# Kernel tuning notes

Measured on AMD Instinct MI355X. Metric: run time of the kernel, lower is better.

The kernel has to match this reference:

```python
import jax, jax.numpy as jnp
import numpy as np

N_TABLES = 26
ROWS = 100001   # n + 1 per EmbeddingBag
D = 64          # m_spa
B = 8192
L = 4           # fixed pooling factor per bag


def setup_inputs() -> dict:
    key = jax.random.key(0)
    ks = jax.random.split(key, 16)
    inp = {}
    inp["dense_x"] = jax.random.normal(ks[0], (B, 13), dtype=jnp.float32)
    # offsets: bag k starts at k*L (fixed pooling factor), same for every table
    inp["lS_o"] = jnp.tile(jnp.arange(B, dtype=jnp.int64) * L, (N_TABLES, 1))
    inp["lS_i"] = jax.random.randint(ks[1], (N_TABLES, B * L), 0, 100000).astype(jnp.int64)
    # embedding tables, uniform(-r, r) with r = sqrt(2/(n+m))
    r = (2.0 / (100000 + D)) ** 0.5
    inp["emb_tables"] = jax.random.uniform(ks[2], (N_TABLES, ROWS, D), dtype=jnp.float32, minval=-r, maxval=r)
    def lin(k, n_in, n_out):
        k1, k2 = jax.random.split(k)
        w = jax.random.normal(k1, (n_out, n_in), dtype=jnp.float32) * (2.0 / n_in) ** 0.5
        b = jax.random.uniform(k2, (n_out,), dtype=jnp.float32, minval=-n_in**-0.5, maxval=n_in**-0.5)
        return w, b
    inp["bot_w0"], inp["bot_b0"] = lin(ks[3], 13, 512)
    inp["bot_w1"], inp["bot_b1"] = lin(ks[4], 512, 256)
    inp["bot_w2"], inp["bot_b2"] = lin(ks[5], 256, 64)
    inp["top_w0"], inp["top_b0"] = lin(ks[6], 415, 512)
    inp["top_w1"], inp["top_b1"] = lin(ks[7], 512, 256)
    inp["top_w2"], inp["top_b2"] = lin(ks[8], 256, 1)
    return inp


def _dlrm(dense_x, lS_o, lS_i, emb_tables,
          bot_w0, bot_b0, bot_w1, bot_b1, bot_w2, bot_b2,
          top_w0, top_b0, top_w1, top_b1, top_w2, top_b2):
    # bottom MLP: Linear+ReLU for every layer (sigmoid_bot=-1)
    x = jax.nn.relu(dense_x @ bot_w0.T + bot_b0)
    x = jax.nn.relu(x @ bot_w1.T + bot_b1)
    x = jax.nn.relu(x @ bot_w2.T + bot_b2)          # [B, D]
    # EmbeddingBag mean pooling per table (fixed bag length L encoded by lS_o)
    idx = lS_i.reshape(N_TABLES, B, L)
    gathered = jax.vmap(lambda tab, ix: tab[ix])(emb_tables, idx)  # [T, B, L, D]
    ly = gathered.mean(axis=2)                       # [T, B, D]
    # dot interaction: T_feat = cat([x]+ly) -> [B, 27, D]
    T_feat = jnp.concatenate([x[None], ly], axis=0).transpose(1, 0, 2)
    Z = jnp.einsum('bnd,bmd->bnm', T_feat, T_feat)   # [B, 27, 27]
    li, lj = np.tril_indices(N_TABLES + 1, -1)       # strict lower triangle (offset=0)
    Zflat = Z[:, li, lj]                             # [B, 351]
    R = jnp.concatenate([x, Zflat], axis=1)          # [B, 415]
    # top MLP: sigmoid_top=2 -> loop breaks before appending Sigmoid -> last layer linear
    z = jax.nn.relu(R @ top_w0.T + top_b0)
    z = jax.nn.relu(z @ top_w1.T + top_b1)
    z = z @ top_w2.T + top_b2                        # [B, 1]
    return z.reshape(-1)


def reference(dense_x, lS_o, lS_i, emb_tables,
              bot_w0, bot_b0, bot_w1, bot_b1, bot_w2, bot_b2,
              top_w0, top_b0, top_w1, top_b1, top_w2, top_b2):
    return _dlrm(dense_x, lS_o, lS_i, emb_tables,
                 bot_w0, bot_b0, bot_w1, bot_b1, bot_w2, bot_b2,
                 top_w0, top_b0, top_w1, top_b1, top_w2, top_b2)
```

## Files before the change

### kernel.cpp

```cpp
#include <hip/hip_runtime.h>
#include <hip/hip_bf16.h>

typedef short bf16x8 __attribute__((ext_vector_type(8)));
typedef float f32x4 __attribute__((ext_vector_type(4)));

__device__ __forceinline__ float relu_f(float v){ return v > 0.f ? v : 0.f; }

__device__ __forceinline__ f32x4 mfma16(bf16x8 a, bf16x8 b, f32x4 c){
  return __builtin_amdgcn_mfma_f32_16x16x32_bf16(a, b, c, 0, 0, 0);
}

__device__ __forceinline__ short bfbits(float v){
  __hip_bfloat16 h = __float2bfloat16(v);
  return *reinterpret_cast<short*>(&h);
}

__global__ __launch_bounds__(256) void prep(
    const float* __restrict__ X,  const float* __restrict__ bw0,
    const float* __restrict__ bb0, __hip_bfloat16* __restrict__ H,
    const float* __restrict__ bw1, __hip_bfloat16* __restrict__ w1b,
    const float* __restrict__ bw2, __hip_bfloat16* __restrict__ w2b,
    const float* __restrict__ tw0, __hip_bfloat16* __restrict__ tw0b,
    const float* __restrict__ tw1, __hip_bfloat16* __restrict__ tw1b){
  int blk = blockIdx.x;
  if (blk < 512){
    int n = threadIdx.x;
    int m0 = blk * 16;
    float w0[13], w1[13];
#pragma unroll
    for (int k = 0; k < 13; k++){ w0[k] = bw0[n*13 + k]; w1[k] = bw0[(n+256)*13 + k]; }
    float b0 = bb0[n], b1 = bb0[n + 256];
    for (int mi = 0; mi < 16; mi++){
      int m = m0 + mi;
      float a0 = b0, a1 = b1;
#pragma unroll
      for (int k = 0; k < 13; k++){
        float xv = X[m*13 + k];
        a0 += xv * w0[k]; a1 += xv * w1[k];
      }
      H[(size_t)m*512 + n]       = __float2bfloat16(relu_f(a0));
      H[(size_t)m*512 + n + 256] = __float2bfloat16(relu_f(a1));
    }
  } else if (blk < 1024){
    int i = (blk - 512)*256 + threadIdx.x;
    w1b[i] = __float2bfloat16(bw1[i]);
  } else if (blk < 1088){
    int i = (blk - 1024)*256 + threadIdx.x;
    w2b[i] = __float2bfloat16(bw2[i]);
  } else if (blk < 1920){
    int i = (blk - 1088)*256 + threadIdx.x;
    int r = i / 416, k = i - r*416;
    float v = (k < 415) ? tw0[r*415 + k] : 0.f;
    tw0b[i] = __float2bfloat16(v);
  } else {
    int i = (blk - 1920)*256 + threadIdx.x;
    tw1b[i] = __float2bfloat16(tw1[i]);
  }
}

template<int NT, int K>
__global__ __launch_bounds__(256) void gemm_br(const __hip_bfloat16* __restrict__ A,
    const __hip_bfloat16* __restrict__ W, const float* __restrict__ Bv,
    __hip_bfloat16* __restrict__ C, int N, int ldc){
  int lane = threadIdx.x & 63;
  int wave = blockIdx.x * 4 + (threadIdx.x >> 6);
  int ntiles = N / (16 * NT);
  int mi = wave / ntiles, ni = wave % ntiles;
  int row = lane & 15, quad = lane >> 4;
  const __hip_bfloat16* Ap = A + (size_t)(mi*16 + row) * K + quad*8;
  const __hip_bfloat16* Wp = W + (size_t)(ni*16*NT + row) * K + quad*8;
  f32x4 acc[NT];
#pragma unroll
  for (int t = 0; t < NT; t++) acc[t] = (f32x4){0.f, 0.f, 0.f, 0.f};
#pragma unroll
  for (int k = 0; k < K; k += 32){
    bf16x8 a = *(const bf16x8*)(Ap + k);
#pragma unroll
    for (int t = 0; t < NT; t++){
      bf16x8 b = *(const bf16x8*)(Wp + (size_t)t*16*K + k);
      acc[t] = mfma16(a, b, acc[t]);
    }
  }
#pragma unroll
  for (int t = 0; t < NT; t++){
    int n = ni*16*NT + t*16 + row;
    float bn = Bv[n];
#pragma unroll
    for (int r = 0; r < 4; r++){
      int m = mi*16 + quad*4 + r;
      C[(size_t)m*ldc + n] = __float2bfloat16(relu_f(acc[t][r] + bn));
    }
  }
}

__global__ __launch_bounds__(256) void embint(const int* __restrict__ I,
    const float* __restrict__ T, __hip_bfloat16* __restrict__ R){
  int b    = blockIdx.x * 4 + (threadIdx.x >> 6);
  int lane = threadIdx.x & 63;
  int row = lane & 15, quad = lane >> 4;
  __hip_bfloat16* Rb = R + (size_t)b * 416;

  int4 ix0 = {0,0,0,0}, ix1 = {0,0,0,0};
  if (row >= 1) ix0 = *(const int4*)(I + ((size_t)(row - 1) << 15) + (b << 2));
  if (row < 11) ix1 = *(const int4*)(I + ((size_t)(row + 15) << 15) + (b << 2));

  f32x4 a00 = {0,0,0,0}, a10 = {0,0,0,0}, a11 = {0,0,0,0};
#pragma unroll
  for (int k = 0; k < 64; k += 32){
    int ko = k + quad*8;
    bf16x8 f0, f1 = {0,0,0,0,0,0,0,0};
    if (row == 0){
      f0 = *(const bf16x8*)(Rb + ko);
    } else {
      const float* tb = T + (size_t)(row - 1) * 6400064ull + ko;
      float s[8] = {0,0,0,0,0,0,0,0};
      int idx[4] = {ix0.x, ix0.y, ix0.z, ix0.w};
#pragma unroll
      for (int l = 0; l < 4; l++){
        const float* p = tb + (size_t)idx[l]*64;
        float4 u = *(const float4*)p;
        float4 v = *(const float4*)(p + 4);
        s[0]+=u.x; s[1]+=u.y; s[2]+=u.z; s[3]+=u.w;
        s[4]+=v.x; s[5]+=v.y; s[6]+=v.z; s[7]+=v.w;
      }
#pragma unroll
      for (int j = 0; j < 8; j++) f0[j] = bfbits(s[j]*0.25f);
    }
    if (row < 11){
      const float* tb = T + (size_t)(row + 15) * 6400064ull + ko;
      float s[8] = {0,0,0,0,0,0,0,0};
      int idx[4] = {ix1.x, ix1.y, ix1.z, ix1.w};
#pragma unroll
      for (int l = 0; l < 4; l++){
        const float* p = tb + (size_t)idx[l]*64;
        float4 u = *(const float4*)p;
        float4 v = *(const float4*)(p + 4);
        s[0]+=u.x; s[1]+=u.y; s[2]+=u.z; s[3]+=u.w;
        s[4]+=v.x; s[5]+=v.y; s[6]+=v.z; s[7]+=v.w;
      }
#pragma unroll
      for (int j = 0; j < 8; j++) f1[j] = bfbits(s[j]*0.25f);
    }
    a00 = mfma16(f0, f0, a00);
    a10 = mfma16(f1, f0, a10);
    a11 = mfma16(f1, f1, a11);
  }
#pragma unroll
  for (int r = 0; r < 4; r++){
    { int i = quad*4 + r, j = row;
      if (i > j) Rb[64 + i*(i-1)/2 + j] = __float2bfloat16(a00[r]); }
    { int i = 16 + quad*4 + r, j = row;
      if (i < 27) Rb[64 + i*(i-1)/2 + j] = __float2bfloat16(a10[r]); }
    { int i = 16 + quad*4 + r, j = 16 + row;
      if (i < 27 && i > j) Rb[64 + i*(i-1)/2 + j] = __float2bfloat16(a11[r]); }
  }
  if (lane == 0) Rb[415] = __float2bfloat16(0.f);
}

template<int K>
__global__ __launch_bounds__(256) void top12(const __hip_bfloat16* __restrict__ A,
    const __hip_bfloat16* __restrict__ W, const float* __restrict__ Bv,
    const float* __restrict__ W2, const float* __restrict__ b2,
    float* __restrict__ O){
  __shared__ float part[4][16];
  int lane = threadIdx.x & 63, wv = threadIdx.x >> 6;
  int mi = blockIdx.x;
  int row = lane & 15, quad = lane >> 4;
  const __hip_bfloat16* Ap = A + (size_t)(mi*16 + row) * K + quad*8;
  int nb = wv * 64;
  const __hip_bfloat16* Wp = W + (size_t)(nb + row) * K + quad*8;
  f32x4 acc[4];
#pragma unroll
  for (int t = 0; t < 4; t++) acc[t] = (f32x4){0.f, 0.f, 0.f, 0.f};
#pragma unroll
  for (int k = 0; k < K; k += 32){
    bf16x8 a = *(const bf16x8*)(Ap + k);
#pragma unroll
    for (int t = 0; t < 4; t++){
      bf16x8 b = *(const bf16x8*)(Wp + (size_t)t*16*K + k);
      acc[t] = mfma16(a, b, acc[t]);
    }
  }
  float p[4];
#pragma unroll
  for (int r = 0; r < 4; r++){
    float s = 0.f;
#pragma unroll
    for (int t = 0; t < 4; t++){
      int n = nb + t*16 + row;
      s += relu_f(acc[t][r] + Bv[n]) * W2[n];
    }
    p[r] = s;
  }
#pragma unroll
  for (int r = 0; r < 4; r++){
#pragma unroll
    for (int o = 1; o < 16; o <<= 1) p[r] += __shfl_xor(p[r], o, 64);
  }
  if (row == 0){
#pragma unroll
    for (int r = 0; r < 4; r++) part[wv][quad*4 + r] = p[r];
  }
  __syncthreads();
  if (threadIdx.x < 16){
    float s = part[0][threadIdx.x] + part[1][threadIdx.x]
            + part[2][threadIdx.x] + part[3][threadIdx.x] + b2[0];
    O[mi*16 + threadIdx.x] = s;
  }
}

extern "C" void kernel_launch(void* const* d_in, const int* in_sizes, int n_in,
                              void* d_out, int out_size, void* d_ws, size_t ws_size,
                              hipStream_t stream) {
  const float* dense_x = (const float*)d_in[0];
  const int*   lS_i    = (const int*)d_in[2];
  const float* tables  = (const float*)d_in[3];
  const float* bw0 = (const float*)d_in[4];  const float* bb0 = (const float*)d_in[5];
  const float* bw1 = (const float*)d_in[6];  const float* bb1 = (const float*)d_in[7];
  const float* bw2 = (const float*)d_in[8];  const float* bb2 = (const float*)d_in[9];
  const float* tw0 = (const float*)d_in[10]; const float* tb0 = (const float*)d_in[11];
  const float* tw1 = (const float*)d_in[12]; const float* tb1 = (const float*)d_in[13];
  const float* tw2 = (const float*)d_in[14]; const float* tb2 = (const float*)d_in[15];
  float* out = (float*)d_out;
  char* ws = (char*)d_ws;

  __hip_bfloat16* w1b  = (__hip_bfloat16*)(ws + 0);
  __hip_bfloat16* w2b  = (__hip_bfloat16*)(ws + 262144);
  __hip_bfloat16* tw0b = (__hip_bfloat16*)(ws + 294912);
  __hip_bfloat16* tw1b = (__hip_bfloat16*)(ws + 720896);
  __hip_bfloat16* h0   = (__hip_bfloat16*)(ws + 983040);
  __hip_bfloat16* h1   = (__hip_bfloat16*)(ws + 9371648);
  __hip_bfloat16* R    = (__hip_bfloat16*)(ws + 13565952);
  __hip_bfloat16* h3   = h0;

  prep<<<2432, 256, 0, stream>>>(dense_x, bw0, bb0, h0,
                                 bw1, w1b, bw2, w2b, tw0, tw0b, tw1, tw1b);
  gemm_br<4,512><<<512, 256, 0, stream>>>(h0, w1b, bb1, h1, 256, 256);
  gemm_br<1,256><<<512, 256, 0, stream>>>(h1, w2b, bb2, R, 64, 416);
  embint<<<8192/4, 256, 0, stream>>>(lS_i, tables, R);
  gemm_br<4,416><<<1024, 256, 0, stream>>>(R, tw0b, tb0, h3, 512, 512);
  top12<512><<<512, 256, 0, stream>>>(h3, tw1b, tb1, tw2, tb2, out);

  (void)in_sizes; (void)n_in; (void)out_size; (void)ws_size;
}
```

Before: 849.0 us.

## Stage embedding bag pooling through LDS with coalesced per-table row gathers

Embedding gathers are restructured so that each wave loads one table at a time. All 64 lanes read consecutive floats of each gathered row, using indices broadcast via readlane, and the pooled means go into shared memory. The MFMA interaction then reads its bf16 fragments from LDS instead of doing scattered 32-byte per-lane gathers. This aims for fully coalesced 256-byte row accesses at the cost of scalar 4-byte loads, a 28KB LDS buffer that can limit occupancy, and a block-wide barrier.

Result: no change. 848.8 us (-0.0%).

```diff
diff --git a/kernel.cpp b/kernel.cpp
--- a/kernel.cpp
+++ b/kernel.cpp
@@ -95,14 +95,32 @@
 
 __global__ __launch_bounds__(256) void embint(const int* __restrict__ I,
     const float* __restrict__ T, __hip_bfloat16* __restrict__ R){
-  int b    = blockIdx.x * 4 + (threadIdx.x >> 6);
+  __shared__ __align__(16) float ly[4][26][68];
+  int wv   = threadIdx.x >> 6;
   int lane = threadIdx.x & 63;
+  int b    = blockIdx.x * 4 + wv;
+  float (*L)[68] = ly[wv];
+
+  int4 myix = (int4){0,0,0,0};
+  if (lane < 26) myix = *(const int4*)(I + ((size_t)lane << 15) + (b << 2));
+
+#pragma unroll
+  for (int t = 0; t < 26; t++){
+    int i0 = __builtin_amdgcn_readlane(myix.x, t);
+    int i1 = __builtin_amdgcn_readlane(myix.y, t);
+    int i2 = __builtin_amdgcn_readlane(myix.z, t);
+    int i3 = __builtin_amdgcn_readlane(myix.w, t);
+    const float* tb = T + (size_t)t * 6400064ull + lane;
+    float s0 = tb[(size_t)(unsigned)i0 * 64];
+    float s1 = tb[(size_t)(unsigned)i1 * 64];
+    float s2 = tb[(size_t)(unsigned)i2 * 64];
+    float s3 = tb[(size_t)(unsigned)i3 * 64];
+    L[t][lane] = (((s0 + s1) + s2) + s3) * 0.25f;
+  }
+  __syncthreads();
+
   int row = lane & 15, quad = lane >> 4;
   __hip_bfloat16* Rb = R + (size_t)b * 416;
-
-  int4 ix0 = {0,0,0,0}, ix1 = {0,0,0,0};
-  if (row >= 1) ix0 = *(const int4*)(I + ((size_t)(row - 1) << 15) + (b << 2));
-  if (row < 11) ix1 = *(const int4*)(I + ((size_t)(row + 15) << 15) + (b << 2));
 
   f32x4 a00 = {0,0,0,0}, a10 = {0,0,0,0}, a11 = {0,0,0,0};
 #pragma unroll
@@ -112,34 +130,14 @@
     if (row == 0){
       f0 = *(const bf16x8*)(Rb + ko);
     } else {
-      const float* tb = T + (size_t)(row - 1) * 6400064ull + ko;
-      float s[8] = {0,0,0,0,0,0,0,0};
-      int idx[4] = {ix0.x, ix0.y, ix0.z, ix0.w};
-#pragma unroll
-      for (int l = 0; l < 4; l++){
-        const float* p = tb + (size_t)idx[l]*64;
-        float4 u = *(const float4*)p;
-        float4 v = *(const float4*)(p + 4);
-        s[0]+=u.x; s[1]+=u.y; s[2]+=u.z; s[3]+=u.w;
-        s[4]+=v.x; s[5]+=v.y; s[6]+=v.z; s[7]+=v.w;
-      }
-#pragma unroll
-      for (int j = 0; j < 8; j++) f0[j] = bfbits(s[j]*0.25f);
+      const float* p = L[row - 1] + ko;
+#pragma unroll
+      for (int j = 0; j < 8; j++) f0[j] = bfbits(p[j]);
     }
     if (row < 11){
-      const float* tb = T + (size_t)(row + 15) * 6400064ull + ko;
-      float s[8] = {0,0,0,0,0,0,0,0};
-      int idx[4] = {ix1.x, ix1.y, ix1.z, ix1.w};
-#pragma unroll
-      for (int l = 0; l < 4; l++){
-        const float* p = tb + (size_t)idx[l]*64;
-        float4 u = *(const float4*)p;
-        float4 v = *(const float4*)(p + 4);
-        s[0]+=u.x; s[1]+=u.y; s[2]+=u.z; s[3]+=u.w;
-        s[4]+=v.x; s[5]+=v.y; s[6]+=v.z; s[7]+=v.w;
-      }
-#pragma unroll
-      for (int j = 0; j < 8; j++) f1[j] = bfbits(s[j]*0.25f);
+      const float* p = L[row + 15] + ko;
+#pragma unroll
+      for (int j = 0; j < 8; j++) f1[j] = bfbits(p[j]);
     }
     a00 = mfma16(f0, f0, a00);
     a10 = mfma16(f1, f0, a10);
```
